# Kernel tuning notes

Measured on AMD Instinct MI355X. Metric: run time of the kernel, lower is better.

## Reference

```python
import jax, jax.numpy as jnp
import numpy as np

TEMPERATURE = 0.0005

def conv1d(x, w, b):
    # x: [B,Cin,T], w: [Cout,Cin,K], 'same' padding as ConvNorm (pad=(K-1)//2)
    pad = (w.shape[-1] - 1) // 2
    y = jax.lax.conv_general_dilated(x, w, window_strides=(1,), padding=[(pad, pad)],
                                     dimension_numbers=('NCH', 'OIH', 'NCH'))
    return y + b[None, :, None]

def setup_inputs() -> dict:
    key = jax.random.key(0)
    ks = jax.random.split(key, 20)
    B, C_MEL, C_TXT, C_ATT, T1, T2 = 32, 80, 512, 80, 1600, 400
    s = 0.02
    return {
        'queries': jax.random.normal(ks[0], (B, C_MEL, T1), jnp.float32),
        'keys': jax.random.normal(ks[1], (B, C_TXT, T2), jnp.float32),
        'mask': jax.random.randint(ks[2], (B, T2, 1), 0, 2).astype(bool),
        'attn_prior': jax.random.uniform(ks[3], (B, T1, T2), jnp.float32),
        'speaker_embed': jax.random.normal(ks[4], (B, C_TXT), jnp.float32),
        # key_proj: Conv(512->1024,k3) -> ReLU -> Conv(1024->80,k1)
        'Wk1': jax.random.normal(ks[5], (C_TXT * 2, C_TXT, 3)) * s,
        'bk1': jax.random.normal(ks[6], (C_TXT * 2,)) * s,
        'Wk2': jax.random.normal(ks[7], (C_ATT, C_TXT * 2, 1)) * s,
        'bk2': jax.random.normal(ks[8], (C_ATT,)) * s,
        # query_proj: Conv(80->160,k3) -> ReLU -> Conv(160->80,k1) -> ReLU -> Conv(80->80,k1)
        'Wq1': jax.random.normal(ks[9], (C_MEL * 2, C_MEL, 3)) * s,
        'bq1': jax.random.normal(ks[10], (C_MEL * 2,)) * s,
        'Wq2': jax.random.normal(ks[11], (C_MEL, C_MEL * 2, 1)) * s,
        'bq2': jax.random.normal(ks[12], (C_MEL,)) * s,
        'Wq3': jax.random.normal(ks[13], (C_ATT, C_MEL, 1)) * s,
        'bq3': jax.random.normal(ks[14], (C_ATT,)) * s,
        # speaker projections (multi_speaker=True)
        'Wks': jax.random.normal(ks[15], (C_TXT, C_TXT)) * s,
        'bks': jax.random.normal(ks[16], (C_TXT,)) * s,
        'Wqs': jax.random.normal(ks[17], (C_MEL, C_TXT)) * s,
        'bqs': jax.random.normal(ks[18], (C_MEL,)) * s,
    }

def reference(queries, keys, mask, attn_prior, speaker_embed,
              Wk1, bk1, Wk2, bk2, Wq1, bq1, Wq2, bq2, Wq3, bq3,
              Wks, bks, Wqs, bqs):
    # speaker conditioning: Linear(spk) broadcast over time, added channelwise
    keys = keys + (speaker_embed @ Wks.T + bks)[:, :, None]
    queries = queries + (speaker_embed @ Wqs.T + bqs)[:, :, None]
    # projections
    k = jax.nn.relu(conv1d(keys, Wk1, bk1))
    k = conv1d(k, Wk2, bk2)                      # [B, C_att, T2]
    q = jax.nn.relu(conv1d(queries, Wq1, bq1))
    q = jax.nn.relu(conv1d(q, Wq2, bq2))
    q = conv1d(q, Wq3, bq3)                      # [B, C_att, T1]
    # -temp * sum_c (q-k)^2 == -temp * (||q||^2 + ||k||^2 - 2 q.k)
    q2 = jnp.sum(q * q, axis=1)                  # [B, T1]
    k2 = jnp.sum(k * k, axis=1)                  # [B, T2]
    qk = jnp.einsum('bct,bcs->bts', q, k)        # [B, T1, T2]
    attn = -TEMPERATURE * (q2[:, :, None] + k2[:, None, :] - 2.0 * qk)
    attn = attn[:, None]                         # [B, 1, T1, T2]
    attn = jax.nn.log_softmax(attn, axis=3) + jnp.log(attn_prior[:, None] + 1e-8)
    attn_logprob = attn
    m = jnp.transpose(mask, (0, 2, 1))[:, :, None, :]  # [B,1,1,T2]
    attn = jnp.where(m, -jnp.inf, attn)
    attn = jax.nn.softmax(attn, axis=3)
    return attn, attn_logprob
```

## Files before the change

kernel.cpp:

```cpp
#include <hip/hip_runtime.h>
#include <math.h>

#define TEMP 0.0005f
#define B_    32
#define CMEL  80
#define CTXT  512
#define T1_   1600
#define T2_   400

typedef short short8 __attribute__((ext_vector_type(8)));
typedef float f32x4 __attribute__((ext_vector_type(4)));

__device__ inline unsigned short f2bf(float f) {
    unsigned u = __float_as_uint(f);
    u += 0x7FFF + ((u >> 16) & 1);
    return (unsigned short)(u >> 16);
}
__device__ inline unsigned pack2(float a, float b) {
    return (unsigned)f2bf(a) | ((unsigned)f2bf(b) << 16);
}

__global__ void bias_kernel(const float* __restrict__ se,
                            const float* __restrict__ Wks, const float* __restrict__ bks,
                            const float* __restrict__ Wqs, const float* __restrict__ bqs,
                            float* __restrict__ kb, float* __restrict__ qb) {
    int tid = blockIdx.x * blockDim.x + threadIdx.x;
    const int nk = B_ * CTXT;
    if (tid < nk) {
        int b = tid / CTXT, c = tid % CTXT;
        const float4* s4 = reinterpret_cast<const float4*>(se + b * CTXT);
        const float4* w4 = reinterpret_cast<const float4*>(Wks + (size_t)c * CTXT);
        float acc = bks[c];
        #pragma unroll 4
        for (int j = 0; j < CTXT / 4; ++j) {
            float4 a = s4[j], w = w4[j];
            acc += a.x * w.x + a.y * w.y + a.z * w.z + a.w * w.w;
        }
        kb[tid] = acc;
    } else if (tid < nk + B_ * CMEL) {
        int t = tid - nk;
        int b = t / CMEL, c = t % CMEL;
        const float4* s4 = reinterpret_cast<const float4*>(se + b * CTXT);
        const float4* w4 = reinterpret_cast<const float4*>(Wqs + (size_t)c * CTXT);
        float acc = bqs[c];
        #pragma unroll 4
        for (int j = 0; j < CTXT / 4; ++j) {
            float4 a = s4[j], w = w4[j];
            acc += a.x * w.x + a.y * w.y + a.z * w.z + a.w * w.w;
        }
        qb[t] = acc;
    }
}

__global__ void cast_weights_kernel(
        const float* __restrict__ Wk1, const float* __restrict__ Wk2,
        const float* __restrict__ Wq1, const float* __restrict__ Wq2,
        const float* __restrict__ Wq3,
        unsigned short* __restrict__ Ab1, unsigned short* __restrict__ A2,
        unsigned short* __restrict__ A3, unsigned short* __restrict__ A4,
        unsigned short* __restrict__ A5) {
    int e = blockIdx.x * 256 + threadIdx.x;
    const int n1 = 1572864, n2 = 81920, n3 = 46080, n4 = 12800, n5 = 7680;
    if (e < n1) {
        int co = e / 1536, rem = e - co * 1536;
        int dt = rem >> 9, ci = rem & 511;
        Ab1[e] = f2bf(Wk1[((size_t)co * 512 + ci) * 3 + dt]);
    } else if ((e -= n1) < n2) {
        A2[e] = f2bf(Wk2[e]);
    } else if ((e -= n2) < n3) {
        int co = e / 288, rem = e - co * 288;
        int dt = rem / 96, cc = rem - dt * 96;
        A3[e] = (cc < 80) ? f2bf(Wq1[((size_t)co * 80 + cc) * 3 + dt]) : 0;
    } else if ((e -= n3) < n4) {
        A4[e] = f2bf(Wq2[e]);
    } else if ((e -= n4) < n5) {
        int co = e / 96, cc = e - co * 96;
        A5[e] = (cc < 80) ? f2bf(Wq3[co * 80 + cc]) : 0;
    }
}

__global__ void castXk_kernel(const float* __restrict__ keys, const float* __restrict__ kb,
                              unsigned short* __restrict__ Xt) {
    __shared__ float tile[64][65];
    const int b = blockIdx.z;
    const int row0 = blockIdx.x * 64;
    const int ci0 = blockIdx.y * 64;
    const int tid = threadIdx.x;
    #pragma unroll
    for (int i = 0; i < 16; ++i) {
        int linear = i * 256 + tid;
        int ci_l = linear >> 6, t_l = linear & 63;
        int t = row0 + t_l - 1;
        float v = 0.f;
        if (t >= 0 && t < 400)
            v = keys[((size_t)b * 512 + ci0 + ci_l) * 400 + t] + kb[b * 512 + ci0 + ci_l];
        tile[t_l][ci_l] = v;
    }
    __syncthreads();
    #pragma unroll
    for (int i = 0; i < 16; ++i) {
        int linear = i * 256 + tid;
        int t_l = linear >> 6, ci_l = linear & 63;
        int row = row0 + t_l;
        if (row < 456)
            Xt[((size_t)b * 456 + row) * 512 + ci0 + ci_l] = f2bf(tile[t_l][ci_l]);
    }
}

__global__ __launch_bounds__(256) void castXq_kernel(
        const float* __restrict__ q, const float* __restrict__ qb,
        unsigned short* __restrict__ Xq1) {
    __shared__ float tile[80][65];
    const int b = blockIdx.y;
    const int t0 = blockIdx.x * 64;
    const int tid = threadIdx.x;
    if (t0 == 0 && tid < 48)
        ((unsigned*)(Xq1 + (size_t)b * 1602 * 96))[tid] = 0u;
    if (t0 == 1536 && tid < 48)
        ((unsigned*)(Xq1 + ((size_t)b * 1602 + 1601) * 96))[tid] = 0u;
    {
        int tl = tid & 63, c0 = tid >> 6;
        for (int c = c0; c < 80; c += 4)
            tile[c][tl] = q[((size_t)b * 80 + c) * 1600 + t0 + tl] + qb[b * 80 + c];
    }
    __syncthreads();
    int row = tid >> 2, cg = tid & 3;
    int t = t0 + row;
    unsigned* orow = (unsigned*)(Xq1 + ((size_t)b * 1602 + t + 1) * 96 + cg * 24);
    #pragma unroll
    for (int jj = 0; jj < 12; ++jj) {
        int c0 = cg * 24 + jj * 2, c1 = c0 + 1;
        float f0 = (c0 < 80) ? tile[c0][row] : 0.f;
        float f1 = (c1 < 80) ? tile[c1][row] : 0.f;
        orow[jj] = pack2(f0, f1);
    }
}

__global__ __launch_bounds__(256) void conv1k_mfma(
        const unsigned short* __restrict__ Ab, const unsigned short* __restrict__ Xt,
        const float* __restrict__ bias, unsigned short* __restrict__ k1c) {
    __shared__ short As[3 * 128 * 40];
    __shared__ short Xs[66 * 40];
    const int b = blockIdx.z;
    const int co0 = blockIdx.y * 128;
    const int t0 = blockIdx.x * 64;
    const int tid = threadIdx.x;
    const int lane = tid & 63, w = tid >> 6;
    const int wm = w >> 1, wn = w & 1;
    const int l15 = lane & 15, quad = lane >> 4;
    f32x4 acc[4][2];
    #pragma unroll
    for (int mt = 0; mt < 4; ++mt)
        #pragma unroll
        for (int nt = 0; nt < 2; ++nt)
            acc[mt][nt] = (f32x4){0.f, 0.f, 0.f, 0.f};

    for (int ci0 = 0; ci0 < 512; ci0 += 32) {
        __syncthreads();
        #pragma unroll
        for (int i = 0; i < 6; ++i) {
            int linear = i * 256 + tid;
            int dt = linear >> 9;
            int rem = linear & 511;
            int r = rem >> 2, c16 = rem & 3;
            int4 v = *(const int4*)(Ab + (size_t)(co0 + r) * 1536 + dt * 512 + ci0 + c16 * 8);
            *(int4*)(As + (dt * 128 + r) * 40 + c16 * 8) = v;
        }
        #pragma unroll
        for (int i = 0; i < 2; ++i) {
            int c = i * 256 + tid;
            if (c < 264) {
                int row = c >> 2, c16 = c & 3;
                int4 v = *(const int4*)(Xt + ((size_t)b * 456 + t0 + row) * 512 + ci0 + c16 * 8);
                *(int4*)(Xs + row * 40 + c16 * 8) = v;
            }
        }
        __syncthreads();
        #pragma unroll
        for (int dt = 0; dt < 3; ++dt) {
            short8 af[4], bfr[2];
            #pragma unroll
            for (int mt = 0; mt < 4; ++mt)
                af[mt] = *(const short8*)(As + (dt * 128 + wm * 64 + mt * 16 + l15) * 40 + quad * 8);
            #pragma unroll
            for (int nt = 0; nt < 2; ++nt)
                bfr[nt] = *(const short8*)(Xs + (wn * 32 + nt * 16 + l15 + dt) * 40 + quad * 8);
            #pragma unroll
            for (int mt = 0; mt < 4; ++mt)
                #pragma unroll
                for (int nt = 0; nt < 2; ++nt)
                    acc[mt][nt] = __builtin_amdgcn_mfma_f32_16x16x32_bf16(af[mt], bfr[nt], acc[mt][nt], 0, 0, 0);
        }
    }
    #pragma unroll
    for (int mt = 0; mt < 4; ++mt) {
        int cob = co0 + wm * 64 + mt * 16 + quad * 4;
        float bv[4];
        #pragma unroll
        for (int r = 0; r < 4; ++r) bv[r] = bias[cob + r];
        #pragma unroll
        for (int nt = 0; nt < 2; ++nt) {
            int t = t0 + wn * 32 + nt * 16 + l15;
            if (t >= 400) continue;
            float v0 = fmaxf(acc[mt][nt][0] + bv[0], 0.f);
            float v1 = fmaxf(acc[mt][nt][1] + bv[1], 0.f);
            float v2 = fmaxf(acc[mt][nt][2] + bv[2], 0.f);
            float v3 = fmaxf(acc[mt][nt][3] + bv[3], 0.f);
            uint2 p;
            p.x = pack2(v0, v1);
            p.y = pack2(v2, v3);
            *(uint2*)(k1c + ((size_t)b * 400 + t) * 1024 + cob) = p;
        }
    }
}

template<int MT, int NKC, int DTC, bool RELU, int OMODE, int INW, int OUTW, int N, int NR>
__global__ __launch_bounds__(256) void gemm_cl(
        const unsigned short* __restrict__ A, const unsigned short* __restrict__ X,
        const float* __restrict__ bias, unsigned short* __restrict__ out) {
    const int b = blockIdx.y;
    const int tid = threadIdx.x;
    const int lane = tid & 63, w = tid >> 6;
    const int l15 = lane & 15, quad = lane >> 4;
    const int s = blockIdx.x * 64 + w * 16 + l15;
    const int srow = (s < N) ? s : (N - 1);
    const unsigned short* xb = X + (size_t)b * NR * INW;

    f32x4 acc[MT];
    #pragma unroll
    for (int mt = 0; mt < MT; ++mt) acc[mt] = (f32x4){0.f, 0.f, 0.f, 0.f};

    #pragma unroll
    for (int kc = 0; kc < NKC; ++kc) {
        const int dt = DTC ? (kc / DTC) : 0;
        const int koff = DTC ? ((kc - dt * DTC) * 32) : (kc * 32);
        short8 bfr = *(const short8*)(xb + (size_t)(srow + dt) * INW + koff + quad * 8);
        #pragma unroll
        for (int mt = 0; mt < MT; ++mt) {
            short8 af = *(const short8*)(A + (size_t)(mt * 16 + l15) * (NKC * 32) + kc * 32 + quad * 8);
            acc[mt] = __builtin_amdgcn_mfma_f32_16x16x32_bf16(af, bfr, acc[mt], 0, 0, 0);
        }
    }
    if (s >= N) return;

    float v[MT][4];
    float ss = 0.f;
    #pragma unroll
    for (int mt = 0; mt < MT; ++mt) {
        #pragma unroll
        for (int r = 0; r < 4; ++r) {
            float x = acc[mt][r] + bias[mt * 16 + quad * 4 + r];
            if (RELU) x = fmaxf(x, 0.f);
            v[mt][r] = x;
            if (OMODE >= 2) ss += x * x;
        }
    }
    if (OMODE >= 2) {
        ss += __shfl_xor(ss, 16, 64);
        ss += __shfl_xor(ss, 32, 64);
    }
    unsigned short* orow = out + ((size_t)b * N + s) * OUTW;
    #pragma unroll
    for (int mt = 0; mt < MT; ++mt) {
        uint2 p;
        p.x = pack2(v[mt][0], v[mt][1]);
        p.y = pack2(v[mt][2], v[mt][3]);
        *(uint2*)(orow + mt * 16 + quad * 4) = p;
    }
    if (OMODE == 1 && quad == 0) {
        uint4 z = {0u, 0u, 0u, 0u};
        *(uint4*)(orow + 80) = z;
        *(uint4*)(orow + 88) = z;
    }
    if (OMODE >= 2 && quad == 0) {
        float e80 = (OMODE == 2) ? (-0.5f * ss) : 1.0f;
        float e81 = (OMODE == 2) ? 1.0f : (-0.5f * ss);
        uint4 z0 = {pack2(e80, e81), 0u, 0u, 0u};
        uint4 z1 = {0u, 0u, 0u, 0u};
        *(uint4*)(orow + 80) = z0;
        *(uint4*)(orow + 88) = z1;
    }
}

__global__ __launch_bounds__(64) void attn_mfma_kernel(
        const unsigned short* __restrict__ qT, const unsigned short* __restrict__ kT,
        const int* __restrict__ mask, const float* __restrict__ prior,
        float* __restrict__ attn_out, float* __restrict__ lp_out) {
    const int b = blockIdx.y;
    const int t10 = blockIdx.x * 16;
    const int lane = threadIdx.x;
    const int l15 = lane & 15, quad = lane >> 4;

    float keep[25];
    #pragma unroll
    for (int ns = 0; ns < 25; ++ns)
        keep[ns] = mask[b * T2_ + ns * 16 + l15] ? 0.f : 1.f;

    const unsigned short* qrow = qT + ((size_t)b * T1_ + t10 + l15) * 96;
    short8 af[3];
    #pragma unroll
    for (int kc = 0; kc < 3; ++kc)
        af[kc] = *(const short8*)(qrow + kc * 32 + quad * 8);

    f32x4 acc[25];
    #pragma unroll
    for (int ns = 0; ns < 25; ++ns) acc[ns] = (f32x4){0.f, 0.f, 0.f, 0.f};
    const unsigned short* kbase = kT + (size_t)b * T2_ * 96 + l15 * 96 + quad * 8;
    #pragma unroll
    for (int ns = 0; ns < 25; ++ns) {
        #pragma unroll
        for (int kc = 0; kc < 3; ++kc) {
            short8 bf = *(const short8*)(kbase + ns * 16 * 96 + kc * 32);
            acc[ns] = __builtin_amdgcn_mfma_f32_16x16x32_bf16(af[kc], bf, acc[ns], 0, 0, 0);
        }
    }

    const float K2T = 2.0f * TEMP;
    #pragma unroll
    for (int r = 0; r < 4; ++r) {
        const int t1 = t10 + quad * 4 + r;
        const float* prow = prior + ((size_t)b * T1_ + t1) * T2_;
        float pe[25];
        #pragma unroll
        for (int ns = 0; ns < 25; ++ns) pe[ns] = prow[ns * 16 + l15] + 1e-8f;

        float l[25];
        #pragma unroll
        for (int ns = 0; ns < 25; ++ns) l[ns] = K2T * acc[ns][r];
        float m = l[0];
        #pragma unroll
        for (int ns = 1; ns < 25; ++ns) m = fmaxf(m, l[ns]);
        #pragma unroll
        for (int off = 1; off <= 8; off <<= 1) m = fmaxf(m, __shfl_xor(m, off, 16));
        float e1[25];
        float sum = 0.f;
        #pragma unroll
        for (int ns = 0; ns < 25; ++ns) { float e = __expf(l[ns] - m); e1[ns] = e; sum += e; }
        #pragma unroll
        for (int off = 1; off <= 8; off <<= 1) sum += __shfl_xor(sum, off, 16);
        const float lse = m + __logf(sum);

        float* lpr = lp_out + ((size_t)b * T1_ + t1) * T2_;
        float* atr = attn_out + ((size_t)b * T1_ + t1) * T2_;
        float u[25];
        float sum2 = 0.f;
        #pragma unroll
        for (int ns = 0; ns < 25; ++ns) {
            float lp = l[ns] - lse + __logf(pe[ns]);
            lpr[ns * 16 + l15] = lp;
            float uu = e1[ns] * pe[ns] * keep[ns];
            u[ns] = uu;
            sum2 += uu;
        }
        #pragma unroll
        for (int off = 1; off <= 8; off <<= 1) sum2 += __shfl_xor(sum2, off, 16);
        const float inv = 1.f / sum2;
        #pragma unroll
        for (int ns = 0; ns < 25; ++ns) atr[ns * 16 + l15] = u[ns] * inv;
    }
}

extern "C" void kernel_launch(void* const* d_in, const int* in_sizes, int n_in,
                              void* d_out, int out_size, void* d_ws, size_t ws_size,
                              hipStream_t stream) {
    const float* queries = (const float*)d_in[0];
    const float* keys    = (const float*)d_in[1];
    const int*   mask    = (const int*)d_in[2];
    const float* prior   = (const float*)d_in[3];
    const float* se      = (const float*)d_in[4];
    const float* Wk1 = (const float*)d_in[5];
    const float* bk1 = (const float*)d_in[6];
    const float* Wk2 = (const float*)d_in[7];
    const float* bk2 = (const float*)d_in[8];
    const float* Wq1 = (const float*)d_in[9];
    const float* bq1 = (const float*)d_in[10];
    const float* Wq2 = (const float*)d_in[11];
    const float* bq2 = (const float*)d_in[12];
    const float* Wq3 = (const float*)d_in[13];
    const float* bq3 = (const float*)d_in[14];
    const float* Wks = (const float*)d_in[15];
    const float* bks = (const float*)d_in[16];
    const float* Wqs = (const float*)d_in[17];
    const float* bqs = (const float*)d_in[18];

    float* ws = (float*)d_ws;
    float* kb = ws;
    float* qb = ws + 16384;
    unsigned short* Ab1 = (unsigned short*)(ws + 18944);
    unsigned short* A2  = (unsigned short*)(ws + 805376);
    unsigned short* A3  = (unsigned short*)(ws + 846336);
    unsigned short* A4  = (unsigned short*)(ws + 869376);
    unsigned short* A5  = (unsigned short*)(ws + 875776);
    unsigned short* qT  = (unsigned short*)(ws + 879616);
    unsigned short* kT  = (unsigned short*)(ws + 3337216);
    const size_t D = 3951616;
    unsigned short* Xk  = (unsigned short*)(ws + D);
    unsigned short* k1c = (unsigned short*)(ws + D + 3735552);
    unsigned short* Xq1 = (unsigned short*)(ws + D);
    unsigned short* Xq2 = (unsigned short*)(ws + D + 2460672);
    unsigned short* Xq3 = (unsigned short*)(ws + D);

    float* attn_out = (float*)d_out;
    float* lp_out   = attn_out + (size_t)B_ * T1_ * T2_;

    bias_kernel<<<dim3(74), dim3(256), 0, stream>>>(se, Wks, bks, Wqs, bqs, kb, qb);
    cast_weights_kernel<<<dim3(6724), dim3(256), 0, stream>>>(Wk1, Wk2, Wq1, Wq2, Wq3,
                                                              Ab1, A2, A3, A4, A5);
    castXk_kernel<<<dim3(8, 8, 32), dim3(256), 0, stream>>>(keys, kb, Xk);
    conv1k_mfma<<<dim3(7, 8, 32), dim3(256), 0, stream>>>(Ab1, Xk, bk1, k1c);
    gemm_cl<5, 32, 0, false, 2, 1024, 96, 400, 400>
        <<<dim3(7, 32), 256, 0, stream>>>(A2, k1c, bk2, kT);
    castXq_kernel<<<dim3(25, 32), dim3(256), 0, stream>>>(queries, qb, Xq1);
    gemm_cl<10, 9, 3, true, 0, 96, 160, 1600, 1602>
        <<<dim3(25, 32), 256, 0, stream>>>(A3, Xq1, bq1, Xq2);
    gemm_cl<5, 5, 0, true, 1, 160, 96, 1600, 1600>
        <<<dim3(25, 32), 256, 0, stream>>>(A4, Xq2, bq2, Xq3);
    gemm_cl<5, 3, 0, false, 3, 96, 96, 1600, 1600>
        <<<dim3(25, 32), 256, 0, stream>>>(A5, Xq3, bq3, qT);
    attn_mfma_kernel<<<dim3(100, 32), dim3(64), 0, stream>>>(qT, kT, mask, prior, attn_out, lp_out);
}
```

Measured before the change: 612.0 us.

## Split attention into MFMA logits kernel and row-wise softmax kernel

The fused attention kernel is split in two. The first kernel computes the scaled q·k logits with MFMA and writes them to workspace as bf16. The second kernel handles one row per wavefront, reading logits, prior and mask with a coalesced lane-contiguous layout and writing both outputs. This is meant to fix the strided, poorly coalesced prior loads and output stores of the fused kernel, and to raise occupancy. The cost is an extra round trip through memory for the logits (about 41 MB) and an added rounding of the logits to bf16 before the softmax.

```diff
diff --git a/kernel.cpp b/kernel.cpp
--- a/kernel.cpp
+++ b/kernel.cpp
@@ -19,6 +19,7 @@
 __device__ inline unsigned pack2(float a, float b) {
     return (unsigned)f2bf(a) | ((unsigned)f2bf(b) << 16);
 }
+__device__ inline float bf2f(unsigned short v) { return __uint_as_float(((unsigned)v) << 16); }
 
 __global__ void bias_kernel(const float* __restrict__ se,
                             const float* __restrict__ Wks, const float* __restrict__ bks,
@@ -282,20 +283,14 @@
     }
 }
 
-__global__ __launch_bounds__(64) void attn_mfma_kernel(
+__global__ __launch_bounds__(64) void attn_logits_kernel(
         const unsigned short* __restrict__ qT, const unsigned short* __restrict__ kT,
-        const int* __restrict__ mask, const float* __restrict__ prior,
-        float* __restrict__ attn_out, float* __restrict__ lp_out) {
+        unsigned short* __restrict__ lgt) {
     const int b = blockIdx.y;
     const int t10 = blockIdx.x * 16;
     const int lane = threadIdx.x;
     const int l15 = lane & 15, quad = lane >> 4;
 
-    float keep[25];
-    #pragma unroll
-    for (int ns = 0; ns < 25; ++ns)
-        keep[ns] = mask[b * T2_ + ns * 16 + l15] ? 0.f : 1.f;
-
     const unsigned short* qrow = qT + ((size_t)b * T1_ + t10 + l15) * 96;
     short8 af[3];
     #pragma unroll
@@ -314,49 +309,71 @@
             acc[ns] = __builtin_amdgcn_mfma_f32_16x16x32_bf16(af[kc], bf, acc[ns], 0, 0, 0);
         }
     }
-
     const float K2T = 2.0f * TEMP;
     #pragma unroll
     for (int r = 0; r < 4; ++r) {
-        const int t1 = t10 + quad * 4 + r;
-        const float* prow = prior + ((size_t)b * T1_ + t1) * T2_;
-        float pe[25];
-        #pragma unroll
-        for (int ns = 0; ns < 25; ++ns) pe[ns] = prow[ns * 16 + l15] + 1e-8f;
-
-        float l[25];
-        #pragma unroll
-        for (int ns = 0; ns < 25; ++ns) l[ns] = K2T * acc[ns][r];
-        float m = l[0];
-        #pragma unroll
-        for (int ns = 1; ns < 25; ++ns) m = fmaxf(m, l[ns]);
-        #pragma unroll
-        for (int off = 1; off <= 8; off <<= 1) m = fmaxf(m, __shfl_xor(m, off, 16));
-        float e1[25];
-        float sum = 0.f;
-        #pragma unroll
-        for (int ns = 0; ns < 25; ++ns) { float e = __expf(l[ns] - m); e1[ns] = e; sum += e; }
-        #pragma unroll
-        for (int off = 1; off <= 8; off <<= 1) sum += __shfl_xor(sum, off, 16);
-        const float lse = m + __logf(sum);
-
-        float* lpr = lp_out + ((size_t)b * T1_ + t1) * T2_;
-        float* atr = attn_out + ((size_t)b * T1_ + t1) * T2_;
-        float u[25];
-        float sum2 = 0.f;
-        #pragma unroll
-        for (int ns = 0; ns < 25; ++ns) {
-            float lp = l[ns] - lse + __logf(pe[ns]);
-            lpr[ns * 16 + l15] = lp;
-            float uu = e1[ns] * pe[ns] * keep[ns];
-            u[ns] = uu;
-            sum2 += uu;
-        }
-        #pragma unroll
-        for (int off = 1; off <= 8; off <<= 1) sum2 += __shfl_xor(sum2, off, 16);
-        const float inv = 1.f / sum2;
-        #pragma unroll
-        for (int ns = 0; ns < 25; ++ns) atr[ns * 16 + l15] = u[ns] * inv;
+        unsigned short* orow = lgt + ((size_t)b * T1_ + t10 + quad * 4 + r) * T2_;
+        #pragma unroll
+        for (int ns = 0; ns < 25; ++ns)
+            orow[ns * 16 + l15] = f2bf(K2T * acc[ns][r]);
+    }
+}
+
+__global__ __launch_bounds__(256) void softmax_kernel(
+        const unsigned short* __restrict__ lgt, const int* __restrict__ mask,
+        const float* __restrict__ prior,
+        float* __restrict__ attn_out, float* __restrict__ lp_out) {
+    const int b = blockIdx.y;
+    const int t1 = blockIdx.x * 4 + (threadIdx.x >> 6);
+    const int lane = threadIdx.x & 63;
+    const unsigned short* lrow = lgt + ((size_t)b * T1_ + t1) * T2_;
+    const float* prow = prior + ((size_t)b * T1_ + t1) * T2_;
+    const int* mrow = mask + b * T2_;
+
+    float l[7], pe[7], kp[7];
+    #pragma unroll
+    for (int j = 0; j < 7; ++j) {
+        int s = lane + 64 * j;
+        bool v = (j < 6) || (lane < 16);
+        l[j]  = v ? bf2f(lrow[s]) : -1e30f;
+        pe[j] = v ? (prow[s] + 1e-8f) : 1.f;
+        kp[j] = (v && !mrow[v ? s : 0]) ? 1.f : 0.f;
+    }
+    float m = l[0];
+    #pragma unroll
+    for (int j = 1; j < 7; ++j) m = fmaxf(m, l[j]);
+    #pragma unroll
+    for (int off = 1; off <= 32; off <<= 1) m = fmaxf(m, __shfl_xor(m, off, 64));
+    float e1[7];
+    float sum = 0.f;
+    #pragma unroll
+    for (int j = 0; j < 7; ++j) { float e = __expf(l[j] - m); e1[j] = e; sum += e; }
+    #pragma unroll
+    for (int off = 1; off <= 32; off <<= 1) sum += __shfl_xor(sum, off, 64);
+    const float lse = m + __logf(sum);
+
+    float u[7];
+    float sum2 = 0.f;
+    #pragma unroll
+    for (int j = 0; j < 7; ++j) {
+        float uu = e1[j] * pe[j] * kp[j];
+        u[j] = uu;
+        sum2 += uu;
+    }
+    #pragma unroll
+    for (int off = 1; off <= 32; off <<= 1) sum2 += __shfl_xor(sum2, off, 64);
+    const float inv = 1.f / sum2;
+
+    float* lpr = lp_out + ((size_t)b * T1_ + t1) * T2_;
+    float* atr = attn_out + ((size_t)b * T1_ + t1) * T2_;
+    #pragma unroll
+    for (int j = 0; j < 7; ++j) {
+        int s = lane + 64 * j;
+        bool v = (j < 6) || (lane < 16);
+        if (v) {
+            lpr[s] = l[j] - lse + __logf(pe[j]);
+            atr[s] = u[j] * inv;
+        }
     }
 }
 
@@ -399,6 +416,7 @@
     unsigned short* Xq1 = (unsigned short*)(ws + D);
     unsigned short* Xq2 = (unsigned short*)(ws + D + 2460672);
     unsigned short* Xq3 = (unsigned short*)(ws + D);
+    unsigned short* lgt = (unsigned short*)(ws + D);
 
     float* attn_out = (float*)d_out;
     float* lp_out   = attn_out + (size_t)B_ * T1_ * T2_;
@@ -417,5 +435,6 @@
         <<<dim3(25, 32), 256, 0, stream>>>(A4, Xq2, bq2, Xq3);
     gemm_cl<5, 3, 0, false, 3, 96, 96, 1600, 1600>
         <<<dim3(25, 32), 256, 0, stream>>>(A5, Xq3, bq3, qT);
-    attn_mfma_kernel<<<dim3(100, 32), dim3(64), 0, stream>>>(qT, kT, mask, prior, attn_out, lp_out);
-}
+    attn_logits_kernel<<<dim3(100, 32), dim3(64), 0, stream>>>(qT, kT, lgt);
+    softmax_kernel<<<dim3(400, 32), dim3(256), 0, stream>>>(lgt, mask, prior, attn_out, lp_out);
+}
```

Measured after the change: 523.7 us. 14.4% less time.
